# Optimization experiments

Hardware: AMD Instinct MI355X
Metric: run time of the kernel (lower is better)

The kernel has to match this reference:

```python
import jax, jax.numpy as jnp
import numpy as np

# AntModel forward, expressed at the ant-count level.
# Original: builds per-batch ragged routing tables where every ant at source
# neuron s is routed by the layer to a destination neuron; counts at each
# destination are accumulated, relu'd, and destinations with zero ants are
# pruned from the table (a no-op on the count vector itself). The deterministic
# layer routing used here is dest[s] = argmax(weights[s, :]).

B = 256
DIMS = [(4096, 4096), (4096, 4096), (4096, 1024)]
MAX_ANTS = 8


def setup_inputs() -> dict:
    key = jax.random.key(0)
    kx, k1, k2, k3 = jax.random.split(key, 4)
    x = jax.random.randint(kx, (B, DIMS[0][0]), 0, MAX_ANTS).astype(jnp.int32)
    W1 = jax.random.normal(k1, DIMS[0], dtype=jnp.float32)
    W2 = jax.random.normal(k2, DIMS[1], dtype=jnp.float32)
    W3 = jax.random.normal(k3, DIMS[2], dtype=jnp.float32)
    return {"x": x, "W1": W1, "W2": W2, "W3": W3}


def _layer(counts, W):
    # counts: [B, n_in] int32 ant counts; W: [n_in, n_out] pheromone weights
    dest = jnp.argmax(W, axis=1)  # [n_in] routing table
    n_out = W.shape[1]
    out = jnp.zeros((counts.shape[0], n_out), dtype=counts.dtype)
    out = out.at[:, dest].add(counts)  # scatter-add counts to destinations
    return jnp.maximum(out, 0)  # layer.relu_func (identity on counts)


def reference(x, W1, W2, W3):
    counts = x.astype(jnp.int32)
    for W in (W1, W2, W3):
        counts = _layer(counts, W)
    return counts.astype(jnp.float32)
```

## Files before the change

kernel.cpp:

```cpp
#include <hip/hip_runtime.h>


#define N_IN   4096
#define N_MID  4096
#define N_OUT  1024
#define BATCH  256

typedef float f4 __attribute__((ext_vector_type(4)));

__device__ __forceinline__ void upd(float v, int idx, float& bv, int& bi) {
    if (v > bv || (v == bv && idx < bi)) { bv = v; bi = idx; }
}

template <int NCOLS>
__device__ __forceinline__ void row_argmax(const float* __restrict__ W, int row,
                                           int* __restrict__ dest) {
    const int lane = threadIdx.x & 63;
    const f4* __restrict__ p =
        reinterpret_cast<const f4*>(W + (size_t)row * NCOLS);
    float bv = -__builtin_huge_valf();
    int bi = 0;
    constexpr int ITERS = NCOLS / 256;
    constexpr int BAT   = (ITERS >= 8) ? 8 : ITERS;
    #pragma unroll
    for (int t0 = 0; t0 < ITERS; t0 += BAT) {
        f4 v[BAT];
        #pragma unroll
        for (int u = 0; u < BAT; ++u)
            v[u] = __builtin_nontemporal_load(p + (size_t)(t0 + u) * 64 + lane);
        __builtin_amdgcn_sched_barrier(0);
        #pragma unroll
        for (int u = 0; u < BAT; ++u) {
            int c = (t0 + u) * 256 + lane * 4;
            upd(v[u].x, c + 0, bv, bi);
            upd(v[u].y, c + 1, bv, bi);
            upd(v[u].z, c + 2, bv, bi);
            upd(v[u].w, c + 3, bv, bi);
        }
    }
    #pragma unroll
    for (int off = 1; off < 64; off <<= 1) {
        float ov = __shfl_xor(bv, off, 64);
        int   oi = __shfl_xor(bi, off, 64);
        if (ov > bv || (ov == bv && oi < bi)) { bv = ov; bi = oi; }
    }
    if (lane == 0) dest[row] = bi;
}

__global__ __launch_bounds__(256) void argmax_all_kernel(
    const float* __restrict__ W1, const float* __restrict__ W2,
    const float* __restrict__ W3, int* __restrict__ dest1,
    int* __restrict__ dest2, int* __restrict__ dest3) {
    const int wave = (blockIdx.x * blockDim.x + threadIdx.x) >> 6;
    if (wave < N_IN) {
        row_argmax<N_MID>(W1, wave, dest1);
    } else if (wave < N_IN + N_MID) {
        row_argmax<N_MID>(W2, wave - N_IN, dest2);
    } else {
        row_argmax<N_OUT>(W3, wave - (N_IN + N_MID), dest3);
    }
}

__global__ __launch_bounds__(1024) void scatter_fused_kernel(
    const int* __restrict__ x, const int* __restrict__ dest1,
    const int* __restrict__ dest2, const int* __restrict__ dest3,
    float* __restrict__ out) {
    __shared__ int fd[N_IN];
    __shared__ int cnt[N_OUT];
    const int b   = blockIdx.x;
    const int tid = threadIdx.x;

    cnt[tid] = 0;
    #pragma unroll
    for (int k = 0; k < N_IN / 1024; ++k) {
        int s = tid + k * 1024;
        fd[s] = dest3[dest2[dest1[s]]];
    }
    __syncthreads();

    const int4 v = reinterpret_cast<const int4*>(x + (size_t)b * N_IN)[tid];
    const int4 d = *reinterpret_cast<const int4*>(&fd[tid * 4]);
    atomicAdd(&cnt[d.x], v.x);
    atomicAdd(&cnt[d.y], v.y);
    atomicAdd(&cnt[d.z], v.z);
    atomicAdd(&cnt[d.w], v.w);
    __syncthreads();
    out[(size_t)b * N_OUT + tid] = (float)cnt[tid];
}

extern "C" void kernel_launch(void* const* d_in, const int* in_sizes, int n_in,
                              void* d_out, int out_size, void* d_ws, size_t ws_size,
                              hipStream_t stream) {
    const int*   x  = (const int*)d_in[0];
    const float* W1 = (const float*)d_in[1];
    const float* W2 = (const float*)d_in[2];
    const float* W3 = (const float*)d_in[3];
    float* out = (float*)d_out;

    int* ws    = (int*)d_ws;
    int* dest1 = ws;
    int* dest2 = ws + N_IN;
    int* dest3 = ws + 2 * N_IN;

    const int total_waves = N_IN + N_MID + N_MID;
    argmax_all_kernel<<<total_waves / 4, 256, 0, stream>>>(W1, W2, W3,
                                                           dest1, dest2, dest3);
    scatter_fused_kernel<<<BATCH, 1024, 0, stream>>>(x, dest1, dest2, dest3, out);
}
```

Measured before the change: 158.4 us.

## Compute argmax only for W2/W3 rows reachable through the routing chain

Splits the single argmax pass into staged kernels. W1 is processed first, then the W2 rows reached by dest1 are marked, then only those rows have their argmax computed. The same is repeated for the W3 rows reached by dest2[dest1]. The intent is to skip reading weight rows that cannot affect the output, cutting memory traffic. In exchange it serializes the layers and adds several small kernel launches.

```diff
diff --git a/kernel.cpp b/kernel.cpp
--- a/kernel.cpp
+++ b/kernel.cpp
@@ -47,18 +47,35 @@
     if (lane == 0) dest[row] = bi;
 }
 
-__global__ __launch_bounds__(256) void argmax_all_kernel(
-    const float* __restrict__ W1, const float* __restrict__ W2,
-    const float* __restrict__ W3, int* __restrict__ dest1,
-    int* __restrict__ dest2, int* __restrict__ dest3) {
-    const int wave = (blockIdx.x * blockDim.x + threadIdx.x) >> 6;
-    if (wave < N_IN) {
-        row_argmax<N_MID>(W1, wave, dest1);
-    } else if (wave < N_IN + N_MID) {
-        row_argmax<N_MID>(W2, wave - N_IN, dest2);
-    } else {
-        row_argmax<N_OUT>(W3, wave - (N_IN + N_MID), dest3);
-    }
+__global__ __launch_bounds__(256) void argmax_w1_kernel(
+    const float* __restrict__ W1, int* __restrict__ dest1,
+    int* __restrict__ used2, int* __restrict__ used3) {
+    const int g = blockIdx.x * 256 + threadIdx.x;
+    if (g < N_MID) used2[g] = 0;
+    else if (g < 2 * N_MID) used3[g - N_MID] = 0;
+    row_argmax<N_MID>(W1, g >> 6, dest1);
+}
+
+__global__ __launch_bounds__(256) void mark2_kernel(
+    const int* __restrict__ dest1, int* __restrict__ used2) {
+    const int g = blockIdx.x * 256 + threadIdx.x;
+    used2[dest1[g]] = 1;
+}
+
+__global__ __launch_bounds__(256) void mark3_kernel(
+    const int* __restrict__ dest1, const int* __restrict__ dest2,
+    int* __restrict__ used3) {
+    const int g = blockIdx.x * 256 + threadIdx.x;
+    used3[dest2[dest1[g]]] = 1;
+}
+
+template <int NCOLS>
+__global__ __launch_bounds__(256) void argmax_pruned_kernel(
+    const float* __restrict__ W, const int* __restrict__ used,
+    int* __restrict__ dest) {
+    const int wave = (blockIdx.x * 256 + threadIdx.x) >> 6;
+    if (!used[wave]) return;
+    row_argmax<NCOLS>(W, wave, dest);
 }
 
 __global__ __launch_bounds__(1024) void scatter_fused_kernel(
@@ -101,9 +118,13 @@
     int* dest1 = ws;
     int* dest2 = ws + N_IN;
     int* dest3 = ws + 2 * N_IN;
+    int* used2 = ws + 3 * N_IN;
+    int* used3 = ws + 4 * N_IN;
 
-    const int total_waves = N_IN + N_MID + N_MID;
-    argmax_all_kernel<<<total_waves / 4, 256, 0, stream>>>(W1, W2, W3,
-                                                           dest1, dest2, dest3);
+    argmax_w1_kernel<<<N_IN / 4, 256, 0, stream>>>(W1, dest1, used2, used3);
+    mark2_kernel<<<N_IN / 256, 256, 0, stream>>>(dest1, used2);
+    argmax_pruned_kernel<N_MID><<<N_MID / 4, 256, 0, stream>>>(W2, used2, dest2);
+    mark3_kernel<<<N_IN / 256, 256, 0, stream>>>(dest1, dest2, used3);
+    argmax_pruned_kernel<N_OUT><<<N_MID / 4, 256, 0, stream>>>(W3, used3, dest3);
     scatter_fused_kernel<<<BATCH, 1024, 0, stream>>>(x, dest1, dest2, dest3, out);
 }
```

Measured after the change: 166.8 us. +5.3%, slower.
